# Optimization experiments

Hardware: AMD Instinct MI355X
Metric: run time of the kernel (lower is better)

Reference implementation:

```python
import jax, jax.numpy as jnp
import numpy as np

B, L, DN, DE, DD, H = 2, 512, 512, 128, 128, 8
DK, DEH, DDH = DN // H, DE // H, DD // H
F = 2 * DK + DEH + 2 * DDH  # per-head concat feature size (176)
SLOPE = 0.2


def _kaiming(key, out_f, in_f):
    bound = np.sqrt(6.0 / ((1.0 + SLOPE ** 2) * in_f))
    return jax.random.uniform(key, (out_f, in_f), minval=-bound, maxval=bound, dtype=jnp.float32)


def lin(x, w, b):
    y = jnp.einsum('...i,oi->...o', x, w)
    return y if b is None else y + b


def setup_inputs() -> dict:
    key = jax.random.key(0)
    ks = jax.random.split(key, 16)
    inp = {
        'node_representation': jax.random.normal(ks[0], (B, L, DN), dtype=jnp.float32),
        'edge_representation': jax.random.normal(ks[1], (B, L, L, DE), dtype=jnp.float32),
        'diff_vec': jax.random.normal(ks[2], (B, L, DD), dtype=jnp.float32),
        'Wn_w': _kaiming(ks[3], DN, DN), 'Wn_b': jnp.zeros((DN,), jnp.float32),
        'We_w': _kaiming(ks[4], DE, DE), 'We_b': jnp.zeros((DE,), jnp.float32),
        'Wd_w': _kaiming(ks[5], DD, DD), 'Wd_b': jnp.zeros((DD,), jnp.float32),
        'Wh_w': _kaiming(ks[6], DK, DK), 'Wh_b': jnp.zeros((DK,), jnp.float32),
        'attn_w': _kaiming(ks[7], 1, F),
        'outn_w': _kaiming(ks[8], DN, DN), 'outn_b': jnp.zeros((DN,), jnp.float32),
        'Wn2_w': _kaiming(ks[9], DN, DN), 'Wn2_b': jnp.zeros((DN,), jnp.float32),
        'We2_w': _kaiming(ks[10], DE, DE), 'We2_b': jnp.zeros((DE,), jnp.float32),
        'Wd2_w': _kaiming(ks[11], DD, DD), 'Wd2_b': jnp.zeros((DD,), jnp.float32),
        'edge_w': _kaiming(ks[12], DEH, F), 'edge_b': jnp.zeros((DEH,), jnp.float32),
        'oute_w': _kaiming(ks[13], DE, DE), 'oute_b': jnp.zeros((DE,), jnp.float32),
    }
    return inp


def reference(node_representation, edge_representation, diff_vec,
              Wn_w, Wn_b, We_w, We_b, Wd_w, Wd_b, Wh_w, Wh_b, attn_w,
              outn_w, outn_b, Wn2_w, Wn2_b, We2_w, We2_b, Wd2_w, Wd2_b,
              edge_w, edge_b, oute_w, oute_b):
    lrelu = lambda x: jax.nn.leaky_relu(x, SLOPE)

    # ---- node update (GAT-style with concat score decomposed per term) ----
    npj = lin(node_representation, Wn_w, Wn_b).reshape(B, L, H, DK)
    epj = lin(edge_representation, We_w, We_b).reshape(B, L, L, H, DEH)
    dpj = lin(diff_vec, Wd_w, Wd_b).reshape(B, L, H, DDH)
    a = attn_w[0]  # concat order: [hi, hj, edge, di, dj]
    a_hi, a_hj = a[:DK], a[DK:2 * DK]
    a_e = a[2 * DK:2 * DK + DEH]
    a_di, a_dj = a[2 * DK + DEH:2 * DK + DEH + DDH], a[-DDH:]
    # scores[b,i,j,h]
    s = (jnp.einsum('blhd,d->blh', npj, a_hi)[:, :, None, :]
         + jnp.einsum('blhd,d->blh', npj, a_hj)[:, None, :, :]
         + jnp.einsum('blmhe,e->blmh', epj, a_e)
         + jnp.einsum('blhd,d->blh', dpj, a_di)[:, :, None, :]
         + jnp.einsum('blhd,d->blh', dpj, a_dj)[:, None, :, :])
    diag = jnp.eye(L, dtype=bool)[None, :, :, None]
    s = jnp.where(diag, -jnp.inf, s)
    probs = jax.nn.softmax(lrelu(s), axis=2)  # softmax over j
    node_wh = lin(npj, Wh_w, Wh_b)  # [B,L,H,DK]
    agg = jnp.einsum('blmh,bmhd->blhd', probs, node_wh)
    new_node = (npj + lrelu(agg)).reshape(B, L, DN)
    new_node = lin(new_node, outn_w, outn_b)

    # ---- edge update (concat-linear decomposed into per-term matmuls) ----
    np2 = lin(new_node, Wn2_w, Wn2_b).reshape(B, L, H, DK)
    ep2 = lin(edge_representation, We2_w, We2_b).reshape(B, L, L, H, DEH)
    dp2 = lin(diff_vec, Wd2_w, Wd2_b).reshape(B, L, H, DDH)
    # edge concat order: [edge, hi, hj, di, dj]
    W_e = edge_w[:, :DEH]
    W_hi = edge_w[:, DEH:DEH + DK]
    W_hj = edge_w[:, DEH + DK:DEH + 2 * DK]
    W_di = edge_w[:, DEH + 2 * DK:DEH + 2 * DK + DDH]
    W_dj = edge_w[:, -DDH:]
    e_out = (jnp.einsum('blmhe,fe->blmhf', ep2, W_e)
             + jnp.einsum('blhd,fd->blhf', np2, W_hi)[:, :, None]
             + jnp.einsum('blhd,fd->blhf', np2, W_hj)[:, None]
             + jnp.einsum('blhd,fd->blhf', dp2, W_di)[:, :, None]
             + jnp.einsum('blhd,fd->blhf', dp2, W_dj)[:, None]
             + edge_b)
    new_edge = lin(e_out.reshape(B, L, L, DE), oute_w, oute_b)
    return new_node, new_edge
```

## Files before the change

### kernel.cpp

```cpp
#include <hip/hip_runtime.h>
#include <hip/hip_bf16.h>

typedef unsigned short u16;
typedef unsigned short u16x8 __attribute__((ext_vector_type(8)));
typedef __bf16 bf16x8 __attribute__((ext_vector_type(8)));
typedef float f32x4 __attribute__((ext_vector_type(4)));

#define LRS 0.2f

__device__ __forceinline__ u16 f2b(float f) {
  __hip_bfloat16 h = __float2bfloat16(f);
  return __builtin_bit_cast(u16, h);
}

template<int K, int O, int KSEG, int R>
__device__ __forceinline__ void gemm_rowsR(const float* xr, const float* W, const float* bias,
                                           float* yl, float* yg, int ygstride) {
  constexpr int KPT = K / KSEG;
  constexpr int OPP = 256 / KSEG;
  const int t = threadIdx.x;
  const int ks = t % KSEG;
  const int oi = t / KSEG;
#pragma unroll
  for (int pass = 0; pass < O / OPP; ++pass) {
    const int o = pass * OPP + oi;
    float a[R];
#pragma unroll
    for (int r = 0; r < R; ++r) a[r] = 0.0f;
    const float* wp = W + (size_t)o * K + ks * KPT;
    const float* xb = xr + ks * KPT;
#pragma unroll 4
    for (int kc = 0; kc < KPT; kc += 4) {
      f32x4 w4 = *(const f32x4*)(wp + kc);
#pragma unroll
      for (int r = 0; r < R; ++r) {
        f32x4 x = *(const f32x4*)(xb + r * K + kc);
#pragma unroll
        for (int j = 0; j < 4; ++j) a[r] += x[j] * w4[j];
      }
    }
#pragma unroll
    for (int d = 1; d < KSEG; d <<= 1)
#pragma unroll
      for (int r = 0; r < R; ++r) a[r] += __shfl_xor(a[r], d, 64);
    if (ks == 0) {
      float bv = bias ? bias[o] : 0.0f;
#pragma unroll
      for (int r = 0; r < R; ++r) {
        float v = a[r] + bv;
        if (yl) yl[r * O + o] = v;
        if (yg) yg[(size_t)r * ygstride + o] = v;
      }
    }
  }
}

__global__ __launch_bounds__(256) void kW1(const float* We_w, const float* We_b, const float* attn,
                                           const float* We2_w, const float* We2_b,
                                           const float* edge_w, const float* edge_b,
                                           float* Mfull, float* vf, float* cbe, float* sconst) {
  int gid = blockIdx.x * 256 + threadIdx.x;
  if (gid < 16384) {
    int hf = gid >> 7, c = gid & 127;
    int h = hf >> 4, fo = hf & 15;
    float s = 0;
    for (int e = 0; e < 16; ++e)
      s += edge_w[fo * 176 + e] * We2_w[(h * 16 + e) * 128 + c];
    Mfull[hf * 128 + c] = s;
  } else if (gid < 16384 + 2048) {
    int idx = gid - 16384;
    int c = idx >> 4, hc = idx & 15;
    if (hc < 8) {
      float s = 0;
      for (int e = 0; e < 16; ++e)
        s += We_w[(hc * 16 + e) * 128 + c] * attn[128 + e];
      vf[c * 8 + hc] = s;
    }
  } else if (gid < 18432 + 128) {
    int hf = gid - 18432;
    int h = hf >> 4, fo = hf & 15;
    float s = edge_b[fo];
    for (int e = 0; e < 16; ++e)
      s += We2_b[h * 16 + e] * edge_w[fo * 176 + e];
    cbe[hf] = s;
  } else if (gid < 18560 + 8) {
    int h = gid - 18560;
    float s = 0;
    for (int e = 0; e < 16; ++e)
      s += We_b[h * 16 + e] * attn[128 + e];
    sconst[h] = s;
  }
}

__global__ __launch_bounds__(256) void kW2(const float* oute_w, const float* Mfull, u16* Gb) {
  int gid = blockIdx.x * 256 + threadIdx.x;
  int o = gid >> 7, c = gid & 127;
  float s = 0;
  for (int k = 0; k < 128; ++k)
    s += oute_w[o * 128 + k] * Mfull[k * 128 + c];
  Gb[o * 128 + c] = f2b(s);
}

__global__ __launch_bounds__(256) void kN1(const float* node, const float* diff,
                                           const float* Wn_w, const float* Wn_b,
                                           const float* Wd_w, const float* Wd_b,
                                           const float* Wh_w, const float* Wh_b,
                                           const float* attn, const float* sconst,
                                           float* npj_g, float* nwh_g,
                                           float* srow_g, float* scol_g) {
  __shared__ float nrow[2 * 512], npjl[2 * 512], drow[2 * 128], dpjl[2 * 128];
  const int t = threadIdx.x;
  const int r0 = blockIdx.x * 2;
  *(f32x4*)&nrow[t * 4] = *(const f32x4*)(node + (size_t)r0 * 512 + t * 4);
  if (t < 64) *(f32x4*)&drow[t * 4] = *(const f32x4*)(diff + (size_t)r0 * 128 + t * 4);
  __syncthreads();
  gemm_rowsR<512, 512, 4, 2>(nrow, Wn_w, Wn_b, npjl, npj_g + (size_t)r0 * 512, 512);
  gemm_rowsR<128, 128, 4, 2>(drow, Wd_w, Wd_b, dpjl, nullptr, 0);
  __syncthreads();
  {
    int d = t & 63, hh = t >> 6;
#pragma unroll
    for (int hi = 0; hi < 2; ++hi) {
      int h = hh + hi * 4;
      float wb = Wh_b[d];
      float acc[2] = {wb, wb};
      for (int k = 0; k < 64; ++k) {
        float w = Wh_w[d * 64 + k];
#pragma unroll
        for (int r = 0; r < 2; ++r) acc[r] += npjl[r * 512 + h * 64 + k] * w;
      }
#pragma unroll
      for (int r = 0; r < 2; ++r) nwh_g[(size_t)(r0 + r) * 512 + h * 64 + d] = acc[r];
    }
  }
  if (t < 16) {
    int r = t >> 3, h = t & 7;
    float shi = 0, shj = 0, sdi = 0, sdj = 0;
    for (int d = 0; d < 64; ++d) {
      float x = npjl[r * 512 + h * 64 + d];
      shi += x * attn[d];
      shj += x * attn[64 + d];
    }
    for (int e = 0; e < 16; ++e) {
      float x = dpjl[r * 128 + h * 16 + e];
      sdi += x * attn[144 + e];
      sdj += x * attn[160 + e];
    }
    srow_g[(r0 + r) * 8 + h] = shi + sdi + sconst[h];
    scol_g[(r0 + r) * 8 + h] = shj + sdj;
  }
}

__global__ __launch_bounds__(256) void kA(const float* edge, const float* npj, const float* nwh,
                                          const float* srow, const float* scol,
                                          const float* vf, float* nnp) {
  __shared__ float sm[4608];
  __shared__ float part[2][512];
  __shared__ float red[256];
  __shared__ float mxh8[8], inv8[8];
  const int bl = blockIdx.x;
  const int b = bl >> 9, l = bl & 511;
  const int t = threadIdx.x;
  const int sub = t & 15, rg = t >> 4;
  const int h = t & 7, seg = t >> 3;

  f32x4 vrx[16];
#pragma unroll
  for (int q = 0; q < 16; ++q) vrx[q] = *(const f32x4*)(vf + sub * 64 + q * 4);

  {
    const float* ebase = edge + ((size_t)bl * 512 + rg) * 128 + sub * 8;
    f32x4 a0v, a1v, b0v, b1v;
    a0v = *(const f32x4*)ebase;          a1v = *(const f32x4*)(ebase + 4);
    b0v = *(const f32x4*)(ebase + 2048); b1v = *(const f32x4*)(ebase + 2052);
#define SCORE_ROW(C0, C1, IT)                                                  \
    {                                                                          \
      float acc[8];                                                            \
      _Pragma("unroll") for (int h2 = 0; h2 < 8; ++h2) acc[h2] = 0.0f;         \
      _Pragma("unroll") for (int j = 0; j < 4; ++j) {                          \
        _Pragma("unroll") for (int h2 = 0; h2 < 8; ++h2) {                     \
          acc[h2] += C0[j] * vrx[j * 2 + (h2 >> 2)][h2 & 3];                   \
          acc[h2] += C1[j] * vrx[8 + j * 2 + (h2 >> 2)][h2 & 3];               \
        }                                                                      \
      }                                                                        \
      _Pragma("unroll") for (int d = 1; d < 16; d <<= 1) {                     \
        _Pragma("unroll") for (int h2 = 0; h2 < 8; ++h2)                       \
          acc[h2] += __shfl_xor(acc[h2], d, 64);                               \
      }                                                                        \
      if (sub < 8) {                                                           \
        float a = acc[0];                                                      \
        _Pragma("unroll") for (int h2 = 1; h2 < 8; ++h2)                       \
          if (sub == h2) a = acc[h2];                                          \
        sm[(IT * 16 + rg) * 9 + sub] = a;                                      \
      }                                                                        \
    }
    for (int it = 0; it < 32; it += 2) {
      SCORE_ROW(a0v, a1v, it);
      if (it + 2 < 32) {
        const float* p = ebase + (size_t)(it + 2) * 2048;
        a0v = *(const f32x4*)p; a1v = *(const f32x4*)(p + 4);
      }
      SCORE_ROW(b0v, b1v, (it + 1));
      if (it + 3 < 32) {
        const float* p = ebase + (size_t)(it + 3) * 2048;
        b0v = *(const f32x4*)p; b1v = *(const f32x4*)(p + 4);
      }
    }
#undef SCORE_ROW
  }
  __syncthreads();
  const float srh2 = srow[(size_t)bl * 8 + h];
  float mx = -__builtin_inff();
#pragma unroll 4
  for (int i = 0; i < 16; ++i) {
    int m = seg * 16 + i;
    float sv = sm[m * 9 + h] + srh2 + scol[((size_t)b * 512 + m) * 8 + h];
    sv = (m == l) ? -__builtin_inff() : (sv >= 0.0f ? sv : LRS * sv);
    sm[m * 9 + h] = sv;
    mx = fmaxf(mx, sv);
  }
  red[t] = mx;
  __syncthreads();
  if (t < 8) {
    float m2 = -__builtin_inff();
    for (int sg = 0; sg < 32; ++sg) m2 = fmaxf(m2, red[sg * 8 + t]);
    mxh8[t] = m2;
  }
  __syncthreads();
  float mh = mxh8[h];
  float smv = 0;
#pragma unroll 4
  for (int i = 0; i < 16; ++i) {
    int m = seg * 16 + i;
    float p = __expf(sm[m * 9 + h] - mh);
    sm[m * 9 + h] = p;
    smv += p;
  }
  red[t] = smv;
  __syncthreads();
  if (t < 8) {
    float s2 = 0;
    for (int sg = 0; sg < 32; ++sg) s2 += red[sg * 8 + t];
    inv8[t] = 1.0f / s2;
  }
  __syncthreads();
  const int half = t >> 7, oq = t & 127;
  const int o4 = oq * 4, hh = oq >> 4;
  f32x4 acc4a = {0, 0, 0, 0}, acc4b = {0, 0, 0, 0};
  const float* nb = nwh + (size_t)b * 512 * 512;
  for (int m = half * 256; m < half * 256 + 256; m += 2) {
    acc4a += sm[m * 9 + hh]       * *(const f32x4*)(nb + (size_t)m * 512 + o4);
    acc4b += sm[(m + 1) * 9 + hh] * *(const f32x4*)(nb + (size_t)(m + 1) * 512 + o4);
  }
  *(f32x4*)&part[half][o4] = acc4a + acc4b;
  __syncthreads();
  if (t < 128) {
    int ob = t * 4, h2 = t >> 4;
    f32x4 s0 = *(f32x4*)&part[0][ob];
    f32x4 s1 = *(f32x4*)&part[1][ob];
    f32x4 np4 = *(const f32x4*)(npj + (size_t)bl * 512 + ob);
    float iv = inv8[h2];
    f32x4 o;
#pragma unroll
    for (int j = 0; j < 4; ++j) {
      float a = (s0[j] + s1[j]) * iv;
      a = a >= 0.0f ? a : LRS * a;
      o[j] = np4[j] + a;
    }
    *(f32x4*)(nnp + (size_t)bl * 512 + ob) = o;
  }
}

__global__ __launch_bounds__(256) void kN234(const float* nnp, const float* diff,
                                             const float* outn_w, const float* outn_b,
                                             const float* Wn2_w, const float* Wn2_b,
                                             const float* Wd2_w, const float* Wd2_b,
                                             const float* edge_w, const float* cbe,
                                             const float* oute_w, const float* oute_b,
                                             float* out0, float* Pl, float* Pm) {
  __shared__ float xr[2 * 512], o0l[2 * 512], np2l[2 * 512], dr[2 * 128], dp2l[2 * 128];
  __shared__ float Rls[2 * 128], Rms[2 * 128];
  const int t = threadIdx.x;
  const int r0 = blockIdx.x * 2;
  *(f32x4*)&xr[t * 4] = *(const f32x4*)(nnp + (size_t)r0 * 512 + t * 4);
  if (t < 64) *(f32x4*)&dr[t * 4] = *(const f32x4*)(diff + (size_t)r0 * 128 + t * 4);
  __syncthreads();
  gemm_rowsR<512, 512, 4, 2>(xr, outn_w, outn_b, o0l, out0 + (size_t)r0 * 512, 512);
  gemm_rowsR<128, 128, 4, 2>(dr, Wd2_w, Wd2_b, dp2l, nullptr, 0);
  __syncthreads();
  gemm_rowsR<512, 512, 4, 2>(o0l, Wn2_w, Wn2_b, np2l, nullptr, 0);
  __syncthreads();
  {
    int hf = t & 127, which = t >> 7;
    int h = hf >> 4, fo = hf & 15;
    const float* wh = edge_w + fo * 176 + 16 + which * 64;
    const float* wd = edge_w + fo * 176 + 144 + which * 16;
    float add = which ? 0.0f : cbe[hf];
    float* dst = which ? Rms : Rls;
#pragma unroll
    for (int r = 0; r < 2; ++r) {
      float a = add;
      for (int d = 0; d < 64; ++d) a += np2l[r * 512 + h * 64 + d] * wh[d];
      for (int e = 0; e < 16; ++e) a += dp2l[r * 128 + h * 16 + e] * wd[e];
      dst[r * 128 + hf] = a;
    }
  }
  __syncthreads();
  gemm_rowsR<128, 128, 4, 2>(Rls, oute_w, oute_b, nullptr, Pl + (size_t)r0 * 128, 128);
  gemm_rowsR<128, 128, 4, 2>(Rms, oute_w, nullptr, nullptr, Pm + (size_t)r0 * 128, 128);
}

__global__ __launch_bounds__(256) void kE(const float* edge, const u16* Gb,
                                          const float* Pl, const float* Pm, float* oute) {
  __shared__ u16 Gt[16384];
  __shared__ u16 At[8192];
  const int tile = blockIdx.x;
  const int bl = tile >> 2;
  const int b = bl >> 9;
  const int q0 = (tile & 3) * 128;
  const int t = threadIdx.x, lane = t & 63, w = t >> 6;
#pragma unroll
  for (int i2 = 0; i2 < 8; ++i2) {
    int u = i2 * 256 + t;
    int row = u >> 4, cu = u & 15;
    *(u16x8*)(Gt + (row * 16 + (cu ^ (row & 7))) * 8) = *(const u16x8*)(Gb + u * 8);
  }
  const int wr = w >> 1, wc = w & 1;
  const int colL = lane & 15, kg = lane >> 4;
  const float* plp = Pl + (size_t)bl * 128;
  f32x4 plv4[4];
#pragma unroll
  for (int n = 0; n < 4; ++n) plv4[n] = *(const f32x4*)(plp + wc * 64 + n * 16 + kg * 4);
  const int arow = t >> 2, aseg = t & 3;

  for (int sub = 0; sub < 2; ++sub) {
    const int r0 = q0 + sub * 64;
    {
      const float* p = edge + ((size_t)bl * 512 + r0 + arow) * 128 + aseg * 32;
      f32x4 v[8];
#pragma unroll
      for (int q = 0; q < 8; ++q) v[q] = *(const f32x4*)(p + q * 4);
#pragma unroll
      for (int jj = 0; jj < 4; ++jj) {
        u16x8 a8;
#pragma unroll
        for (int j2 = 0; j2 < 4; ++j2) {
          a8[j2]     = f2b(v[2 * jj][j2]);
          a8[4 + j2] = f2b(v[2 * jj + 1][j2]);
        }
        int cu = aseg * 4 + jj;
        *(u16x8*)(At + (arow * 16 + (cu ^ (arow & 7))) * 8) = a8;
      }
    }
    __syncthreads();
    f32x4 acc[2][4] = {};
#pragma unroll
    for (int ks = 0; ks < 4; ++ks) {
      int cu = ks * 4 + kg;
      bf16x8 af[2], bfv[4];
#pragma unroll
      for (int i = 0; i < 2; ++i) {
        int row = wr * 32 + i * 16 + colL;
        af[i] = *(bf16x8*)(At + (row * 16 + (cu ^ (row & 7))) * 8);
      }
#pragma unroll
      for (int n = 0; n < 4; ++n) {
        int orow = wc * 64 + n * 16 + colL;
        bfv[n] = *(bf16x8*)(Gt + (orow * 16 + (cu ^ (orow & 7))) * 8);
      }
#pragma unroll
      for (int i = 0; i < 2; ++i)
#pragma unroll
        for (int n = 0; n < 4; ++n)
          acc[i][n] = __builtin_amdgcn_mfma_f32_16x16x32_bf16(bfv[n], af[i], acc[i][n], 0, 0, 0);
    }
    float* ob = oute + ((size_t)bl * 512 + r0) * 128;
#pragma unroll
    for (int i = 0; i < 2; ++i) {
      int m = wr * 32 + i * 16 + colL;
      const float* pmp = Pm + ((size_t)b * 512 + r0 + m) * 128;
      float* orow = ob + (size_t)m * 128;
#pragma unroll
      for (int n = 0; n < 4; ++n) {
        int oc = wc * 64 + n * 16 + kg * 4;
        f32x4 pm4 = *(const f32x4*)(pmp + oc);
        f32x4 o4;
#pragma unroll
        for (int r = 0; r < 4; ++r) o4[r] = acc[i][n][r] + plv4[n][r] + pm4[r];
        *(f32x4*)(orow + oc) = o4;
      }
    }
    __syncthreads();
  }
}

extern "C" void kernel_launch(void* const* d_in, const int* in_sizes, int n_in,
                              void* d_out, int out_size, void* d_ws, size_t ws_size,
                              hipStream_t stream) {
  (void)in_sizes; (void)n_in; (void)out_size; (void)ws_size;
  const float* node   = (const float*)d_in[0];
  const float* edge   = (const float*)d_in[1];
  const float* diff   = (const float*)d_in[2];
  const float* Wn_w   = (const float*)d_in[3];
  const float* Wn_b   = (const float*)d_in[4];
  const float* We_w   = (const float*)d_in[5];
  const float* We_b   = (const float*)d_in[6];
  const float* Wd_w   = (const float*)d_in[7];
  const float* Wd_b   = (const float*)d_in[8];
  const float* Wh_w   = (const float*)d_in[9];
  const float* Wh_b   = (const float*)d_in[10];
  const float* attn   = (const float*)d_in[11];
  const float* outn_w = (const float*)d_in[12];
  const float* outn_b = (const float*)d_in[13];
  const float* Wn2_w  = (const float*)d_in[14];
  const float* Wn2_b  = (const float*)d_in[15];
  const float* We2_w  = (const float*)d_in[16];
  const float* We2_b  = (const float*)d_in[17];
  const float* Wd2_w  = (const float*)d_in[18];
  const float* Wd2_b  = (const float*)d_in[19];
  const float* edge_w = (const float*)d_in[20];
  const float* edge_b = (const float*)d_in[21];
  const float* oute_w = (const float*)d_in[22];
  const float* oute_b = (const float*)d_in[23];

  float* out0 = (float*)d_out;
  float* out1 = out0 + 524288;

  float* f = (float*)d_ws;
  size_t off = 0;
  auto alloc = [&](size_t n) { float* p = f + off; off += (n + 7) & ~(size_t)7; return p; };
  float* npj    = alloc(524288);
  float* nwh    = alloc(524288);
  float* srow   = alloc(8192);
  float* scol   = alloc(8192);
  float* sconst = alloc(8);
  float* cbe    = alloc(128);
  float* Mfull  = alloc(16384);
  float* nnp    = alloc(524288);
  float* Pl     = alloc(131072);
  float* Pm     = alloc(131072);
  float* vf     = alloc(1024);
  u16* Gb = (u16*)(f + off); off += 8192;

  hipLaunchKernelGGL(kW1, dim3(73), dim3(256), 0, stream,
                     We_w, We_b, attn, We2_w, We2_b, edge_w, edge_b, Mfull, vf, cbe, sconst);
  hipLaunchKernelGGL(kW2, dim3(64), dim3(256), 0, stream, oute_w, Mfull, Gb);
  hipLaunchKernelGGL(kN1, dim3(512), dim3(256), 0, stream,
                     node, diff, Wn_w, Wn_b, Wd_w, Wd_b, Wh_w, Wh_b, attn, sconst,
                     npj, nwh, srow, scol);
  hipLaunchKernelGGL(kA, dim3(1024), dim3(256), 0, stream,
                     edge, npj, nwh, srow, scol, vf, nnp);
  hipLaunchKernelGGL(kN234, dim3(512), dim3(256), 0, stream,
                     nnp, diff, outn_w, outn_b, Wn2_w, Wn2_b, Wd2_w, Wd2_b,
                     edge_w, cbe, oute_w, oute_b, out0, Pl, Pm);
  hipLaunchKernelGGL(kE, dim3(4096), dim3(256), 0, stream, edge, Gb, Pl, Pm, out1);
}
```

Before: 458.7 us.

## Use MFMA for attention edge scores and cache bf16 edge tiles for edge GEMM

```diff
diff --git a/kernel.cpp b/kernel.cpp
--- a/kernel.cpp
+++ b/kernel.cpp
@@ -58,7 +58,7 @@
 __global__ __launch_bounds__(256) void kW1(const float* We_w, const float* We_b, const float* attn,
                                            const float* We2_w, const float* We2_b,
                                            const float* edge_w, const float* edge_b,
-                                           float* Mfull, float* vf, float* cbe, float* sconst) {
+                                           float* Mfull, u16* vb, float* cbe, float* sconst) {
   int gid = blockIdx.x * 256 + threadIdx.x;
   if (gid < 16384) {
     int hf = gid >> 7, c = gid & 127;
@@ -70,12 +70,11 @@
   } else if (gid < 16384 + 2048) {
     int idx = gid - 16384;
     int c = idx >> 4, hc = idx & 15;
-    if (hc < 8) {
-      float s = 0;
+    float s = 0;
+    if (hc < 8)
       for (int e = 0; e < 16; ++e)
         s += We_w[(hc * 16 + e) * 128 + c] * attn[128 + e];
-      vf[c * 8 + hc] = s;
-    }
+    vb[c * 16 + hc] = f2b(s);
   } else if (gid < 18432 + 128) {
     int hf = gid - 18432;
     int h = hf >> 4, fo = hf & 15;
@@ -153,7 +152,8 @@
 
 __global__ __launch_bounds__(256) void kA(const float* edge, const float* npj, const float* nwh,
                                           const float* srow, const float* scol,
-                                          const float* vf, float* nnp) {
+                                          const u16* vb, float* nnp, u16* abf) {
+  __shared__ u16 At[8192];
   __shared__ float sm[4608];
   __shared__ float part[2][512];
   __shared__ float red[256];
@@ -161,54 +161,60 @@
   const int bl = blockIdx.x;
   const int b = bl >> 9, l = bl & 511;
   const int t = threadIdx.x;
-  const int sub = t & 15, rg = t >> 4;
+  const int lane = t & 63, w = t >> 6;
+  const int colL = lane & 15, kg = lane >> 4;
   const int h = t & 7, seg = t >> 3;
-
-  f32x4 vrx[16];
-#pragma unroll
-  for (int q = 0; q < 16; ++q) vrx[q] = *(const f32x4*)(vf + sub * 64 + q * 4);
-
-  {
-    const float* ebase = edge + ((size_t)bl * 512 + rg) * 128 + sub * 8;
-    f32x4 a0v, a1v, b0v, b1v;
-    a0v = *(const f32x4*)ebase;          a1v = *(const f32x4*)(ebase + 4);
-    b0v = *(const f32x4*)(ebase + 2048); b1v = *(const f32x4*)(ebase + 2052);
-#define SCORE_ROW(C0, C1, IT)                                                  \
-    {                                                                          \
-      float acc[8];                                                            \
-      _Pragma("unroll") for (int h2 = 0; h2 < 8; ++h2) acc[h2] = 0.0f;         \
-      _Pragma("unroll") for (int j = 0; j < 4; ++j) {                          \
-        _Pragma("unroll") for (int h2 = 0; h2 < 8; ++h2) {                     \
-          acc[h2] += C0[j] * vrx[j * 2 + (h2 >> 2)][h2 & 3];                   \
-          acc[h2] += C1[j] * vrx[8 + j * 2 + (h2 >> 2)][h2 & 3];               \
-        }                                                                      \
-      }                                                                        \
-      _Pragma("unroll") for (int d = 1; d < 16; d <<= 1) {                     \
-        _Pragma("unroll") for (int h2 = 0; h2 < 8; ++h2)                       \
-          acc[h2] += __shfl_xor(acc[h2], d, 64);                               \
-      }                                                                        \
-      if (sub < 8) {                                                           \
-        float a = acc[0];                                                      \
-        _Pragma("unroll") for (int h2 = 1; h2 < 8; ++h2)                       \
-          if (sub == h2) a = acc[h2];                                          \
-        sm[(IT * 16 + rg) * 9 + sub] = a;                                      \
-      }                                                                        \
-    }
-    for (int it = 0; it < 32; it += 2) {
-      SCORE_ROW(a0v, a1v, it);
-      if (it + 2 < 32) {
-        const float* p = ebase + (size_t)(it + 2) * 2048;
-        a0v = *(const f32x4*)p; a1v = *(const f32x4*)(p + 4);
-      }
-      SCORE_ROW(b0v, b1v, (it + 1));
-      if (it + 3 < 32) {
-        const float* p = ebase + (size_t)(it + 3) * 2048;
-        b0v = *(const f32x4*)p; b1v = *(const f32x4*)(p + 4);
-      }
-    }
-#undef SCORE_ROW
-  }
-  __syncthreads();
+  const int arow = t >> 2, aseg = t & 3;
+
+  bf16x8 bfr[4];
+#pragma unroll
+  for (int ks = 0; ks < 4; ++ks) {
+    u16x8 u;
+#pragma unroll
+    for (int j = 0; j < 8; ++j) u[j] = vb[(ks * 32 + kg * 8 + j) * 16 + colL];
+    bfr[ks] = __builtin_bit_cast(bf16x8, u);
+  }
+
+  for (int tl = 0; tl < 8; ++tl) {
+    {
+      const float* p = edge + ((size_t)bl * 512 + tl * 64 + arow) * 128 + aseg * 32;
+      f32x4 v[8];
+#pragma unroll
+      for (int q = 0; q < 8; ++q) v[q] = *(const f32x4*)(p + q * 4);
+      u16* dst = abf ? abf + ((size_t)bl * 8 + tl) * 8192 : nullptr;
+#pragma unroll
+      for (int jj = 0; jj < 4; ++jj) {
+        u16x8 a8;
+#pragma unroll
+        for (int j2 = 0; j2 < 4; ++j2) {
+          a8[j2]     = f2b(v[2 * jj][j2]);
+          a8[4 + j2] = f2b(v[2 * jj + 1][j2]);
+        }
+        int cu = aseg * 4 + jj;
+        int su = arow * 16 + (cu ^ (arow & 7));
+        *(u16x8*)(At + su * 8) = a8;
+        if (dst) *(u16x8*)(dst + su * 8) = a8;
+      }
+    }
+    __syncthreads();
+    f32x4 acc = {0, 0, 0, 0};
+#pragma unroll
+    for (int ks = 0; ks < 4; ++ks) {
+      int cu = ks * 4 + kg;
+      int lrow = w * 16 + colL;
+      bf16x8 af = *(bf16x8*)(At + (lrow * 16 + (cu ^ (lrow & 7))) * 8);
+      acc = __builtin_amdgcn_mfma_f32_16x16x32_bf16(af, bfr[ks], acc, 0, 0, 0);
+    }
+    if (colL < 8) {
+#pragma unroll
+      for (int r = 0; r < 4; ++r) {
+        int m = tl * 64 + w * 16 + kg * 4 + r;
+        sm[m * 9 + colL] = acc[r];
+      }
+    }
+    __syncthreads();
+  }
+
   const float srh2 = srow[(size_t)bl * 8 + h];
   float mx = -__builtin_inff();
 #pragma unroll 4
@@ -310,8 +316,8 @@
   gemm_rowsR<128, 128, 4, 2>(Rms, oute_w, nullptr, nullptr, Pm + (size_t)r0 * 128, 128);
 }
 
-__global__ __launch_bounds__(256) void kE(const float* edge, const u16* Gb,
-                                          const float* Pl, const float* Pm, float* oute) {
+__global__ __launch_bounds__(256) void kEc(const u16* Abf, const u16* Gb,
+                                           const float* Pl, const float* Pm, float* oute) {
   __shared__ u16 Gt[16384];
   __shared__ u16 At[8192];
   const int tile = blockIdx.x;
@@ -331,6 +337,77 @@
   f32x4 plv4[4];
 #pragma unroll
   for (int n = 0; n < 4; ++n) plv4[n] = *(const f32x4*)(plp + wc * 64 + n * 16 + kg * 4);
+
+  for (int sub = 0; sub < 2; ++sub) {
+    const int r0 = q0 + sub * 64;
+    const int gs = (tile & 3) * 2 + sub;
+    const u16* src = Abf + ((size_t)bl * 8 + gs) * 8192;
+#pragma unroll
+    for (int q = 0; q < 4; ++q)
+      *(u16x8*)(At + q * 2048 + t * 8) = *(const u16x8*)(src + q * 2048 + t * 8);
+    __syncthreads();
+    f32x4 acc[2][4] = {};
+#pragma unroll
+    for (int ks = 0; ks < 4; ++ks) {
+      int cu = ks * 4 + kg;
+      bf16x8 af[2], bfv[4];
+#pragma unroll
+      for (int i = 0; i < 2; ++i) {
+        int row = wr * 32 + i * 16 + colL;
+        af[i] = *(bf16x8*)(At + (row * 16 + (cu ^ (row & 7))) * 8);
+      }
+#pragma unroll
+      for (int n = 0; n < 4; ++n) {
+        int orow = wc * 64 + n * 16 + colL;
+        bfv[n] = *(bf16x8*)(Gt + (orow * 16 + (cu ^ (orow & 7))) * 8);
+      }
+#pragma unroll
+      for (int i = 0; i < 2; ++i)
+#pragma unroll
+        for (int n = 0; n < 4; ++n)
+          acc[i][n] = __builtin_amdgcn_mfma_f32_16x16x32_bf16(bfv[n], af[i], acc[i][n], 0, 0, 0);
+    }
+    float* ob = oute + ((size_t)bl * 512 + r0) * 128;
+#pragma unroll
+    for (int i = 0; i < 2; ++i) {
+      int m = wr * 32 + i * 16 + colL;
+      const float* pmp = Pm + ((size_t)b * 512 + r0 + m) * 128;
+      float* orow = ob + (size_t)m * 128;
+#pragma unroll
+      for (int n = 0; n < 4; ++n) {
+        int oc = wc * 64 + n * 16 + kg * 4;
+        f32x4 pm4 = *(const f32x4*)(pmp + oc);
+        f32x4 o4;
+#pragma unroll
+        for (int r = 0; r < 4; ++r) o4[r] = acc[i][n][r] + plv4[n][r] + pm4[r];
+        *(f32x4*)(orow + oc) = o4;
+      }
+    }
+    __syncthreads();
+  }
+}
+
+__global__ __launch_bounds__(256) void kEd(const float* edge, const u16* Gb,
+                                           const float* Pl, const float* Pm, float* oute) {
+  __shared__ u16 Gt[16384];
+  __shared__ u16 At[8192];
+  const int tile = blockIdx.x;
+  const int bl = tile >> 2;
+  const int b = bl >> 9;
+  const int q0 = (tile & 3) * 128;
+  const int t = threadIdx.x, lane = t & 63, w = t >> 6;
+#pragma unroll
+  for (int i2 = 0; i2 < 8; ++i2) {
+    int u = i2 * 256 + t;
+    int row = u >> 4, cu = u & 15;
+    *(u16x8*)(Gt + (row * 16 + (cu ^ (row & 7))) * 8) = *(const u16x8*)(Gb + u * 8);
+  }
+  const int wr = w >> 1, wc = w & 1;
+  const int colL = lane & 15, kg = lane >> 4;
+  const float* plp = Pl + (size_t)bl * 128;
+  f32x4 plv4[4];
+#pragma unroll
+  for (int n = 0; n < 4; ++n) plv4[n] = *(const f32x4*)(plp + wc * 64 + n * 16 + kg * 4);
   const int arow = t >> 2, aseg = t & 3;
 
   for (int sub = 0; sub < 2; ++sub) {
@@ -397,7 +474,7 @@
 extern "C" void kernel_launch(void* const* d_in, const int* in_sizes, int n_in,
                               void* d_out, int out_size, void* d_ws, size_t ws_size,
                               hipStream_t stream) {
-  (void)in_sizes; (void)n_in; (void)out_size; (void)ws_size;
+  (void)in_sizes; (void)n_in; (void)out_size;
   const float* node   = (const float*)d_in[0];
   const float* edge   = (const float*)d_in[1];
   const float* diff   = (const float*)d_in[2];
@@ -439,19 +516,25 @@
   float* nnp    = alloc(524288);
   float* Pl     = alloc(131072);
   float* Pm     = alloc(131072);
-  float* vf     = alloc(1024);
+  u16* vb = (u16*)(f + off); off += 1024;
   u16* Gb = (u16*)(f + off); off += 8192;
+  const size_t abf_elems = (size_t)2 * 512 * 512 * 128;
+  bool cache = ws_size >= off * 4 + abf_elems * 2 + 256;
+  u16* Abf = cache ? (u16*)(f + off) : nullptr;
 
   hipLaunchKernelGGL(kW1, dim3(73), dim3(256), 0, stream,
-                     We_w, We_b, attn, We2_w, We2_b, edge_w, edge_b, Mfull, vf, cbe, sconst);
+                     We_w, We_b, attn, We2_w, We2_b, edge_w, edge_b, Mfull, vb, cbe, sconst);
   hipLaunchKernelGGL(kW2, dim3(64), dim3(256), 0, stream, oute_w, Mfull, Gb);
   hipLaunchKernelGGL(kN1, dim3(512), dim3(256), 0, stream,
                      node, diff, Wn_w, Wn_b, Wd_w, Wd_b, Wh_w, Wh_b, attn, sconst,
                      npj, nwh, srow, scol);
   hipLaunchKernelGGL(kA, dim3(1024), dim3(256), 0, stream,
-                     edge, npj, nwh, srow, scol, vf, nnp);
+                     edge, npj, nwh, srow, scol, vb, nnp, Abf);
   hipLaunchKernelGGL(kN234, dim3(512), dim3(256), 0, stream,
                      nnp, diff, outn_w, outn_b, Wn2_w, Wn2_b, Wd2_w, Wd2_b,
                      edge_w, cbe, oute_w, oute_b, out0, Pl, Pm);
-  hipLaunchKernelGGL(kE, dim3(4096), dim3(256), 0, stream, edge, Gb, Pl, Pm, out1);
-}
+  if (cache)
+    hipLaunchKernelGGL(kEc, dim3(4096), dim3(256), 0, stream, Abf, Gb, Pl, Pm, out1);
+  else
+    hipLaunchKernelGGL(kEd, dim3(4096), dim3(256), 0, stream, edge, Gb, Pl, Pm, out1);
+}
```

New measurement: 474.5 us. +3.5%, slower.
